# Kernel optimization log

Hardware: AMD Instinct MI355X
Metric: run time of the kernel (lower is better)

The kernel has to match this reference:

```python
import jax, jax.numpy as jnp
import numpy as np

BN_EPS = 1e-5
POOL_TARGETS = (1500, 750, 375)


def mesh_conv(x, nb, W, g, b):
    # x: (E, C), nb: (E, 4), W: (5*C, Cout)
    E, C = x.shape
    n = x[jnp.clip(nb, 0, E - 1)]              # (E, 4, C) gather
    p1 = jnp.sort(n[:, :2, :], axis=1)          # symmetrize face-pair 1
    p2 = jnp.sort(n[:, 2:, :], axis=1)          # symmetrize face-pair 2
    feat = jnp.concatenate([x, p1[:, 0], p1[:, 1], p2[:, 0], p2[:, 1]], axis=1)  # (E, 5C)
    h = feat @ W                                # (E, Cout)
    mu = h.mean(axis=0)
    var = h.var(axis=0)                         # biased var (BatchNorm training stats)
    h = (h - mu) * jax.lax.rsqrt(var + BN_EPS) * g + b
    return jax.nn.relu(h)


def mesh_pool(x, nb, target):
    E = x.shape[0]
    scores = jnp.linalg.norm(x, axis=1)
    keep = jnp.sort(jnp.argsort(-scores)[:target])          # (target,) sorted kept edges
    x_pool = x[keep]
    remap = jnp.full((E,), -1, dtype=jnp.int32).at[keep].set(jnp.arange(target, dtype=jnp.int32))
    nbr = remap[jnp.clip(nb[keep], 0, E - 1)]               # (target, 4)
    self_idx = jnp.broadcast_to(jnp.arange(target, dtype=jnp.int32)[:, None], nbr.shape)
    nb_pool = jnp.where(nbr < 0, self_idx, nbr)
    return x_pool, nb_pool, keep


def mesh_unpool(x_coarse, keep, E_fine):
    # keep is sorted ascending; nearest kept edge by integer index distance
    # (ties -> lower index, matching torch argmin-first semantics).
    idx = jnp.arange(E_fine)
    pos = jnp.searchsorted(keep, idx)
    K = keep.shape[0]
    left = jnp.clip(pos - 1, 0, K - 1)
    right = jnp.clip(pos, 0, K - 1)
    dl = jnp.abs(idx - keep[left])
    dr = jnp.abs(idx - keep[right])
    nn_idx = jnp.where(dl <= dr, left, right)
    return x_coarse[nn_idx]                                 # kept edges map to themselves (d=0)


def setup_inputs() -> dict:
    key = jax.random.key(0)
    ks = jax.random.split(key, 20)
    E = 200000
    x = jax.random.normal(ks[0], (E, 5), dtype=jnp.float32)
    nb = jax.random.randint(ks[1], (E, 4), 0, E, dtype=jnp.int64)

    def lin(k, cin, cout):
        return (jax.random.normal(k, (cin, cout), dtype=jnp.float32) * 0.05)

    dims = [(5, 64), (64, 128), (128, 256), (256, 512), (768, 256), (384, 128), (192, 64)]
    names = ['e1', 'e2', 'e3', 'e4', 'd3', 'd2', 'd1']
    inp = {'x': x, 'nb': nb}
    for i, ((cin, cout), nm) in enumerate(zip(dims, names)):
        inp['W_' + nm] = lin(ks[2 + i], cin * 5, cout)
        inp['g_' + nm] = jnp.ones((cout,), dtype=jnp.float32)
        inp['b_' + nm] = jnp.zeros((cout,), dtype=jnp.float32)
    inp['W_head'] = lin(ks[12], 64, 4)
    inp['bias_head'] = jnp.zeros((4,), dtype=jnp.float32)
    return inp


def _forward(x, nb,
             W_e1, g_e1, b_e1, W_e2, g_e2, b_e2, W_e3, g_e3, b_e3, W_e4, g_e4, b_e4,
             W_d3, g_d3, b_d3, W_d2, g_d2, b_d2, W_d1, g_d1, b_d1,
             W_head, bias_head):
    e1 = mesh_conv(x, nb, W_e1, g_e1, b_e1)
    e1p, nb1, keep1 = mesh_pool(e1, nb, POOL_TARGETS[0])
    e2 = mesh_conv(e1p, nb1, W_e2, g_e2, b_e2)
    e2p, nb2, keep2 = mesh_pool(e2, nb1, POOL_TARGETS[1])
    e3 = mesh_conv(e2p, nb2, W_e3, g_e3, b_e3)
    e3p, nb3, keep3 = mesh_pool(e3, nb2, POOL_TARGETS[2])
    e4 = mesh_conv(e3p, nb3, W_e4, g_e4, b_e4)
    d3 = mesh_unpool(e4, keep3, e3.shape[0])
    d3 = mesh_conv(jnp.concatenate([d3, e3], axis=1), nb2, W_d3, g_d3, b_d3)
    d2 = mesh_unpool(d3, keep2, e2.shape[0])
    d2 = mesh_conv(jnp.concatenate([d2, e2], axis=1), nb1, W_d2, g_d2, b_d2)
    d1 = mesh_unpool(d2, keep1, e1.shape[0])
    d1 = mesh_conv(jnp.concatenate([d1, e1], axis=1), nb, W_d1, g_d1, b_d1)
    return d1 @ W_head + bias_head


def reference(x, nb,
              W_e1, g_e1, b_e1, W_e2, g_e2, b_e2, W_e3, g_e3, b_e3, W_e4, g_e4, b_e4,
              W_d3, g_d3, b_d3, W_d2, g_d2, b_d2, W_d1, g_d1, b_d1,
              W_head, bias_head):
    return _forward(x, nb,
                    W_e1, g_e1, b_e1, W_e2, g_e2, b_e2, W_e3, g_e3, b_e3, W_e4, g_e4, b_e4,
                    W_d3, g_d3, b_d3, W_d2, g_d2, b_d2, W_d1, g_d1, b_d1,
                    W_head, bias_head)
```

## Files before the change

### kernel.cpp

```cpp
#include <hip/hip_runtime.h>
#include <stdint.h>

typedef unsigned long long u64;
typedef unsigned int u32;
typedef unsigned short ushort_t;

#define FI __device__ __forceinline__

static constexpr float BN_EPS_F = 1e-5f;
static constexpr int E0 = 200000;
static constexpr int T1 = 1500, T2 = 750, T3 = 375;
static constexpr int CAND_CAP = 4096;
static constexpr int NB_KEEP = (E0 + 1023) / 1024;

typedef __attribute__((ext_vector_type(8))) short short8;
typedef __attribute__((ext_vector_type(4))) float f32x4;

FI int iclampi(int v, int lo, int hi) { return v < lo ? lo : (v > hi ? hi : v); }

FI ushort_t f2b(float f) {
  u32 u = __float_as_uint(f);
  u32 r = (u + 0x7FFFu + ((u >> 16) & 1u)) >> 16;
  return (ushort_t)r;
}

FI int nearest_keep(const int* __restrict__ keep, int K, int idx) {
  int lo = 0, hi = K;
  while (lo < hi) { int mid = (lo + hi) >> 1; if (keep[mid] < idx) lo = mid + 1; else hi = mid; }
  int l = lo - 1; l = l < 0 ? 0 : (l > K - 1 ? K - 1 : l);
  int r = lo;     r = r < 0 ? 0 : (r > K - 1 ? K - 1 : r);
  int dl = idx - keep[l]; dl = dl < 0 ? -dl : dl;
  int dr = idx - keep[r]; dr = dr < 0 ? -dr : dr;
  return (dl <= dr) ? l : r;
}

FI int bsearch_eq(const int* __restrict__ keep, int K, int v) {
  int lo = 0, hi = K;
  while (lo < hi) { int mid = (lo + hi) >> 1; if (keep[mid] < v) lo = mid + 1; else hi = mid; }
  if (lo < K && keep[lo] == v) return lo;
  return -1;
}

template<int C, int Cout, int BR, int BC, int KT, int TR, int TC, int KSPLIT,
         bool FUSE_STATS>
__global__ __launch_bounds__((BR / TR) * (BC / TC))
void conv_kernel(const float* __restrict__ X,
                 const int* __restrict__ nb, int E,
                 const float* __restrict__ W,
                 float* __restrict__ H, float* __restrict__ stats)
{
  constexpr int NTH = (BR / TR) * (BC / TC);
  constexpr int VK = 5 * KT;
  constexpr int KC = C / KSPLIT;
  static_assert(KC % KT == 0, "KC % KT");

  const int row0 = blockIdx.x * BR;
  const int col0 = blockIdx.y * BC;
  const int c_begin = (KSPLIT > 1) ? (int)blockIdx.z * KC : 0;

  __shared__ float As[VK][BR];
  __shared__ float Bs[VK][BC];
  __shared__ int rowsS[5][BR];
  __shared__ float red[FUSE_STATS ? 2 * (BR / TR) * BC : 1];

  const int tid = threadIdx.x;

  for (int q = tid; q < BR; q += NTH) {
    int r = row0 + q;
    int rr[5];
    if (r < E) {
      rr[0] = r;
      #pragma unroll
      for (int j = 0; j < 4; j++) {
        int v = nb[(size_t)r * 4 + j];
        rr[1 + j] = iclampi(v, 0, E - 1);
      }
    } else {
      #pragma unroll
      for (int j = 0; j < 5; j++) rr[j] = -1;
    }
    #pragma unroll
    for (int j = 0; j < 5; j++) rowsS[j][q] = rr[j];
  }

  float acc[TR][TC];
  #pragma unroll
  for (int i = 0; i < TR; i++)
    #pragma unroll
    for (int j = 0; j < TC; j++) acc[i][j] = 0.f;

  const int tr = tid / (BC / TC);
  const int tc = tid % (BC / TC);
  const int rA = tr * TR;
  const int cB = tc * TC;

  for (int c0 = c_begin; c0 < c_begin + KC; c0 += KT) {
    __syncthreads();
    for (int q = tid; q < VK * (BC / 4); q += NTH) {
      int kk = q / (BC / 4);
      int c4 = q % (BC / 4);
      int p = kk / KT, t = kk % KT;
      float4 wv = *(const float4*)&W[(size_t)(p * C + c0 + t) * Cout + col0 + c4 * 4];
      *(float4*)&Bs[kk][c4 * 4] = wv;
    }
    for (int q = tid; q < BR * KT; q += NTH) {
      int t = q % KT, rq = q / KT;
      int c = c0 + t;
      float s0 = 0.f, a1 = 0.f, a2 = 0.f, a3 = 0.f, a4 = 0.f;
      if (rowsS[0][rq] >= 0) {
        float v0, v1, v2, v3;
        s0 = X[(size_t)rowsS[0][rq] * C + c];
        v0 = X[(size_t)rowsS[1][rq] * C + c];
        v1 = X[(size_t)rowsS[2][rq] * C + c];
        v2 = X[(size_t)rowsS[3][rq] * C + c];
        v3 = X[(size_t)rowsS[4][rq] * C + c];
        a1 = fminf(v0, v1); a2 = fmaxf(v0, v1);
        a3 = fminf(v2, v3); a4 = fmaxf(v2, v3);
      }
      As[0 * KT + t][rq] = s0;
      As[1 * KT + t][rq] = a1;
      As[2 * KT + t][rq] = a2;
      As[3 * KT + t][rq] = a3;
      As[4 * KT + t][rq] = a4;
    }
    __syncthreads();

    for (int kk = 0; kk < VK; kk++) {
      float a[TR], b[TC];
      #pragma unroll
      for (int i = 0; i < TR; i++) a[i] = As[kk][rA + i];
      #pragma unroll
      for (int j = 0; j < TC; j++) b[j] = Bs[kk][cB + j];
      #pragma unroll
      for (int i = 0; i < TR; i++)
        #pragma unroll
        for (int j = 0; j < TC; j++)
          acc[i][j] = fmaf(a[i], b[j], acc[i][j]);
    }
  }

  #pragma unroll
  for (int i = 0; i < TR; i++) {
    int r = row0 + rA + i;
    if (r < E) {
      if constexpr (KSPLIT > 1) {
        #pragma unroll
        for (int j = 0; j < TC; j++)
          atomicAdd(&H[(size_t)r * Cout + col0 + cB + j], acc[i][j]);
      } else {
        #pragma unroll
        for (int j = 0; j < TC; j += 4) {
          float4 v = make_float4(acc[i][j], acc[i][j + 1], acc[i][j + 2], acc[i][j + 3]);
          *(float4*)&H[(size_t)r * Cout + col0 + cB + j] = v;
        }
      }
    }
  }

  if constexpr (FUSE_STATS) {
    float s[TC], q2[TC];
    #pragma unroll
    for (int j = 0; j < TC; j++) { s[j] = 0.f; q2[j] = 0.f; }
    #pragma unroll
    for (int i = 0; i < TR; i++) {
      int r = row0 + rA + i;
      if (r < E) {
        #pragma unroll
        for (int j = 0; j < TC; j++) { float v = acc[i][j]; s[j] += v; q2[j] += v * v; }
      }
    }
    __syncthreads();
    float* redS = &red[0];
    float* redQ = &red[(BR / TR) * BC];
    #pragma unroll
    for (int j = 0; j < TC; j++) {
      redS[tr * BC + cB + j] = s[j];
      redQ[tr * BC + cB + j] = q2[j];
    }
    __syncthreads();
    for (int col = tid; col < BC; col += NTH) {
      float ts = 0.f, tq = 0.f;
      for (int g = 0; g < BR / TR; g++) { ts += redS[g * BC + col]; tq += redQ[g * BC + col]; }
      atomicAdd(&stats[col0 + col], ts);
      atomicAdd(&stats[Cout + col0 + col], tq);
    }
  }
}

__global__ __launch_bounds__(256, 4)
void d1_mfma_kernel(const ushort_t* __restrict__ d2b, const ushort_t* __restrict__ e1b,
                    const int* __restrict__ nn1, const int* __restrict__ nb,
                    const ushort_t* __restrict__ Wt,
                    float* __restrict__ H, float* __restrict__ stats)
{
  __shared__ int rowsD[5][128];
  __shared__ int rowsS[5][128];

  const int tid = threadIdx.x;
  const int lane = tid & 63;
  const int wv = tid >> 6;
  const int l15 = lane & 15;
  const int quad = lane >> 4;
  const int row0 = (int)blockIdx.x * 128;

  if (tid < 128) {
    int r = row0 + tid; if (r > E0 - 1) r = E0 - 1;
    int rs[5];
    rs[0] = r;
    #pragma unroll
    for (int j = 0; j < 4; j++) rs[1 + j] = iclampi((int)nb[(size_t)r * 4 + j], 0, E0 - 1);
    #pragma unroll
    for (int j = 0; j < 5; j++) { rowsS[j][tid] = rs[j]; rowsD[j][tid] = nn1[rs[j]]; }
  }
  __syncthreads();

  f32x4 acc[8];
  #pragma unroll
  for (int mi = 0; mi < 8; mi++) acc[mi] = (f32x4){0.f, 0.f, 0.f, 0.f};

  for (int cc = 0; cc < 6; cc++) {
    const bool fromD = cc < 4;
    const ushort_t* __restrict__ src = fromD ? d2b : e1b;
    const int stride = fromD ? 128 : 64;
    const int cbase = (fromD ? cc * 32 : (cc - 4) * 32) + quad * 8;

    short8 bf[5];
    #pragma unroll
    for (int p = 0; p < 5; p++)
      bf[p] = *(const short8*)&Wt[((size_t)(p * 64 + wv * 16 + l15)) * 192 + cc * 32 + quad * 8];

    #pragma unroll 2
    for (int mi = 0; mi < 8; mi++) {
      int rr = mi * 16 + l15;
      int r0, r1, r2, r3, r4;
      if (fromD) {
        r0 = rowsD[0][rr]; r1 = rowsD[1][rr]; r2 = rowsD[2][rr];
        r3 = rowsD[3][rr]; r4 = rowsD[4][rr];
      } else {
        r0 = rowsS[0][rr]; r1 = rowsS[1][rr]; r2 = rowsS[2][rr];
        r3 = rowsS[3][rr]; r4 = rowsS[4][rr];
      }
      uint4 v0 = *(const uint4*)&src[(size_t)r0 * stride + cbase];
      uint4 v1 = *(const uint4*)&src[(size_t)r1 * stride + cbase];
      uint4 v2 = *(const uint4*)&src[(size_t)r2 * stride + cbase];
      uint4 v3 = *(const uint4*)&src[(size_t)r3 * stride + cbase];
      uint4 v4 = *(const uint4*)&src[(size_t)r4 * stride + cbase];

      uint4 lo12, hi12, lo34, hi34;
      {
        const ushort_t* a = (const ushort_t*)&v1;
        const ushort_t* b = (const ushort_t*)&v2;
        ushort_t* lo = (ushort_t*)&lo12;
        ushort_t* hi = (ushort_t*)&hi12;
        #pragma unroll
        for (int i = 0; i < 8; i++) {
          ushort_t x = a[i], y = b[i];
          lo[i] = x < y ? x : y;
          hi[i] = x < y ? y : x;
        }
      }
      {
        const ushort_t* a = (const ushort_t*)&v3;
        const ushort_t* b = (const ushort_t*)&v4;
        ushort_t* lo = (ushort_t*)&lo34;
        ushort_t* hi = (ushort_t*)&hi34;
        #pragma unroll
        for (int i = 0; i < 8; i++) {
          ushort_t x = a[i], y = b[i];
          lo[i] = x < y ? x : y;
          hi[i] = x < y ? y : x;
        }
      }
      acc[mi] = __builtin_amdgcn_mfma_f32_16x16x32_bf16(*(short8*)&v0,   bf[0], acc[mi], 0, 0, 0);
      acc[mi] = __builtin_amdgcn_mfma_f32_16x16x32_bf16(*(short8*)&lo12, bf[1], acc[mi], 0, 0, 0);
      acc[mi] = __builtin_amdgcn_mfma_f32_16x16x32_bf16(*(short8*)&hi12, bf[2], acc[mi], 0, 0, 0);
      acc[mi] = __builtin_amdgcn_mfma_f32_16x16x32_bf16(*(short8*)&lo34, bf[3], acc[mi], 0, 0, 0);
      acc[mi] = __builtin_amdgcn_mfma_f32_16x16x32_bf16(*(short8*)&hi34, bf[4], acc[mi], 0, 0, 0);
    }
  }

  const int col = wv * 16 + l15;
  float s = 0.f, q = 0.f;
  #pragma unroll
  for (int mi = 0; mi < 8; mi++) {
    #pragma unroll
    for (int reg = 0; reg < 4; reg++) {
      int r = row0 + mi * 16 + quad * 4 + reg;
      if (r < E0) {
        float v = acc[mi][reg];
        H[(size_t)r * 64 + col] = v;
        s += v; q += v * v;
      }
    }
  }
  s += __shfl_xor(s, 16); q += __shfl_xor(q, 16);
  s += __shfl_xor(s, 32); q += __shfl_xor(q, 32);
  if (quad == 0) {
    atomicAdd(&stats[col], s);
    atomicAdd(&stats[64 + col], q);
  }
}

__global__ void prep_wd1_kernel(const float* __restrict__ W, ushort_t* __restrict__ Wt)
{
  int idx = (int)blockIdx.x * 256 + threadIdx.x;
  if (idx < 5 * 64 * 192) {
    int n = idx & 63;
    int k = idx >> 6;
    int p = k / 192, c = k % 192;
    Wt[((size_t)(p * 64 + n)) * 192 + c] = f2b(W[(size_t)k * 64 + n]);
  }
}

__global__ void stats_kernel(const float* __restrict__ H, int E, int Cout,
                             float* __restrict__ stats)
{
  const int RB = 64;
  int r0 = (int)blockIdx.x * RB;
  int rend = r0 + RB; if (rend > E) rend = E;
  for (int col = threadIdx.x; col < Cout; col += blockDim.x) {
    float s = 0.f, q = 0.f;
    for (int r = r0; r < rend; r++) { float v = H[(size_t)r * Cout + col]; s += v; q += v * v; }
    atomicAdd(&stats[col], s);
    atomicAdd(&stats[Cout + col], q);
  }
}

template<int Cout, bool KEYS, bool B16>
__global__ void bn_kernel(const float* __restrict__ H, const float* __restrict__ stats,
                          const float* __restrict__ g, const float* __restrict__ b,
                          int E, float* __restrict__ Out, ushort_t* __restrict__ Outb,
                          u64* __restrict__ keys)
{
  constexpr int CPL = Cout / 64;
  const int lane = threadIdx.x & 63;
  const int wid = threadIdx.x >> 6;
  const int wpb = blockDim.x >> 6;
  const float invE = 1.0f / (float)E;
  float mu[CPL], inv[CPL], gg[CPL], bb[CPL];
  #pragma unroll
  for (int u = 0; u < CPL; u++) {
    int c = lane + u * 64;
    float m = stats[c] * invE;
    float var = stats[Cout + c] * invE - m * m;
    mu[u] = m;
    inv[u] = rsqrtf(var + BN_EPS_F);
    gg[u] = g[c]; bb[u] = b[c];
  }
  for (int r = (int)blockIdx.x * wpb + wid; r < E; r += (int)gridDim.x * wpb) {
    float ss = 0.f;
    #pragma unroll
    for (int u = 0; u < CPL; u++) {
      int c = lane + u * 64;
      float v = H[(size_t)r * Cout + c];
      float o = (v - mu[u]) * inv[u] * gg[u] + bb[u];
      o = fmaxf(o, 0.f);
      Out[(size_t)r * Cout + c] = o;
      if constexpr (B16) Outb[(size_t)r * Cout + c] = f2b(o);
      ss += o * o;
    }
    if constexpr (KEYS) {
      #pragma unroll
      for (int s = 32; s > 0; s >>= 1) ss += __shfl_xor(ss, s, 64);
      if (lane == 0) {
        float sc = sqrtf(ss);
        u32 sb = __float_as_uint(sc);
        keys[r] = ((u64)sb << 32) | (u64)(0xFFFFFFFFu - (u32)r);
      }
    }
  }
}

__global__ void head_kernel(const float* __restrict__ H, const float* __restrict__ stats,
                            const float* __restrict__ g, const float* __restrict__ b,
                            const float* __restrict__ Wh, const float* __restrict__ bh,
                            int E, float* __restrict__ out)
{
  const int lane = threadIdx.x & 63;
  const int wid = threadIdx.x >> 6;
  const int wpb = blockDim.x >> 6;
  const float invE = 1.0f / (float)E;
  float m = stats[lane] * invE;
  float var = stats[64 + lane] * invE - m * m;
  float inv = rsqrtf(var + BN_EPS_F);
  float gg = g[lane], bb = b[lane];
  float4 w = *(const float4*)&Wh[lane * 4];
  float b0 = bh[0], b1 = bh[1], b2 = bh[2], b3 = bh[3];
  for (int r = (int)blockIdx.x * wpb + wid; r < E; r += (int)gridDim.x * wpb) {
    float v = H[(size_t)r * 64 + lane];
    float o = fmaxf((v - m) * inv * gg + bb, 0.f);
    float a0 = o * w.x, a1 = o * w.y, a2 = o * w.z, a3 = o * w.w;
    #pragma unroll
    for (int s = 32; s > 0; s >>= 1) {
      a0 += __shfl_xor(a0, s, 64);
      a1 += __shfl_xor(a1, s, 64);
      a2 += __shfl_xor(a2, s, 64);
      a3 += __shfl_xor(a3, s, 64);
    }
    if (lane == 0) {
      float4 ov = make_float4(a0 + b0, a1 + b1, a2 + b2, a3 + b3);
      *(float4*)&out[(size_t)r * 4] = ov;
    }
  }
}

__global__ void hist_kernel(const u64* __restrict__ keys, int E, u32* __restrict__ hist)
{
  for (int i = (int)blockIdx.x * blockDim.x + threadIdx.x; i < E;
       i += (int)gridDim.x * blockDim.x) {
    u32 bin = (u32)(keys[i] >> 44);
    atomicAdd(&hist[bin], 1u);
  }
}

__global__ void scan_kernel(const u32* __restrict__ hist, int K, u32* __restrict__ sel)
{
  __shared__ u32 csum[1024];
  __shared__ int selChunk;
  __shared__ u32 aboveChunk;
  const int tid = threadIdx.x;
  u32 s = 0;
  const u32* hp = hist + (size_t)tid * 1024;
  for (int i = 0; i < 1024; i++) s += hp[i];
  csum[tid] = s;
  __syncthreads();
  if (tid == 0) {
    u32 above = 0; int sc = 0; u32 ab = 0;
    for (int t = 1023; t >= 0; t--) {
      if (above + csum[t] >= (u32)K) { sc = t; ab = above; break; }
      above += csum[t];
    }
    selChunk = sc; aboveChunk = ab;
  }
  __syncthreads();
  if (tid == 0) {
    u32 above = aboveChunk; int sb = 0;
    const u32* hq = hist + (size_t)selChunk * 1024;
    for (int t = 1023; t >= 0; t--) {
      u32 c = hq[t];
      if (above + c >= (u32)K) { sb = t; break; }
      above += c;
    }
    sel[0] = (u32)(selChunk * 1024 + sb);
    sel[1] = above;
    sel[2] = (u32)K - above;
  }
}

__global__ void collect_kernel(const u64* __restrict__ keys, int E, const u32* __restrict__ sel,
                               u64* __restrict__ cand, u32* __restrict__ count)
{
  u32 bin = sel[0];
  for (int i = (int)blockIdx.x * blockDim.x + threadIdx.x; i < E;
       i += (int)gridDim.x * blockDim.x) {
    if ((u32)(keys[i] >> 44) == bin) {
      u32 p = atomicAdd(count, 1u);
      if (p < (u32)CAND_CAP) cand[p] = keys[i];
    }
  }
}

__global__ void thresh_kernel(const u64* __restrict__ cand, const u32* __restrict__ count,
                              const u32* __restrict__ sel, u64* __restrict__ thr)
{
  __shared__ u64 sk[CAND_CAP];
  const int tid = threadIdx.x;
  const int nth = blockDim.x;
  int n = (int)(*count > (u32)CAND_CAP ? (u32)CAND_CAP : *count);
  int n2 = 2; while (n2 < n) n2 <<= 1;
  for (int i = tid; i < n2; i += nth) sk[i] = (i < n) ? cand[i] : 0ull;
  __syncthreads();
  for (int k = 2; k <= n2; k <<= 1)
    for (int j = k >> 1; j > 0; j >>= 1) {
      for (int i = tid; i < n2; i += nth) {
        int p = i ^ j;
        if (p > i) {
          u64 a = sk[i], bb = sk[p];
          bool up = ((i & k) == 0);
          bool sw = up ? (a < bb) : (a > bb);
          if (sw) { sk[i] = bb; sk[p] = a; }
        }
      }
      __syncthreads();
    }
  if (tid == 0) {
    int kr = (int)sel[2];
    thr[0] = sk[kr - 1];
  }
}

__global__ void keep_count_kernel(const u64* __restrict__ keys, int E,
                                  const u64* __restrict__ thrp, u32* __restrict__ bcnt)
{
  const u64 thr = thrp[0];
  const int tid = threadIdx.x;
  int base = (int)blockIdx.x * 1024 + tid * 4;
  u32 c = 0;
  #pragma unroll
  for (int u = 0; u < 4; u++) {
    int i = base + u;
    if (i < E && keys[i] >= thr) c++;
  }
  __shared__ u32 sm[256];
  sm[tid] = c;
  __syncthreads();
  for (int s = 128; s > 0; s >>= 1) {
    if (tid < s) sm[tid] += sm[tid + s];
    __syncthreads();
  }
  if (tid == 0) bcnt[blockIdx.x] = sm[0];
}

__global__ void keep_scan_kernel(const u32* __restrict__ bcnt, int NB, u32* __restrict__ boffs)
{
  __shared__ u32 sm[256];
  const int tid = threadIdx.x;
  u32 v = (tid < NB) ? bcnt[tid] : 0;
  sm[tid] = v;
  __syncthreads();
  for (int off = 1; off < 256; off <<= 1) {
    u32 t = 0;
    if (tid >= off) t = sm[tid - off];
    __syncthreads();
    sm[tid] += t;
    __syncthreads();
  }
  if (tid < NB) boffs[tid] = sm[tid] - v;
}

__global__ void keep_scatter_kernel(const u64* __restrict__ keys, int E,
                                    const u64* __restrict__ thrp, const u32* __restrict__ boffs,
                                    int* __restrict__ keep, int K)
{
  const u64 thr = thrp[0];
  const int tid = threadIdx.x;
  int base = (int)blockIdx.x * 1024 + tid * 4;
  u32 f[4]; u32 c = 0;
  #pragma unroll
  for (int u = 0; u < 4; u++) {
    int i = base + u;
    f[u] = (i < E && keys[i] >= thr) ? 1u : 0u;
    c += f[u];
  }
  __shared__ u32 sm[256];
  sm[tid] = c;
  __syncthreads();
  for (int off = 1; off < 256; off <<= 1) {
    u32 t = 0;
    if (tid >= off) t = sm[tid - off];
    __syncthreads();
    sm[tid] += t;
    __syncthreads();
  }
  u32 pos = boffs[blockIdx.x] + sm[tid] - c;
  #pragma unroll
  for (int u = 0; u < 4; u++) {
    if (f[u]) {
      if (pos < (u32)K) keep[pos] = base + u;
      pos++;
    }
  }
}

template<int NPOW>
__global__ void pool_select_kernel(const u64* __restrict__ keys, int E, int K,
                                   int* __restrict__ keep)
{
  __shared__ u64 sk[NPOW];
  __shared__ int si[NPOW];
  const int tid = threadIdx.x, nth = blockDim.x;
  for (int i = tid; i < NPOW; i += nth) sk[i] = (i < E) ? keys[i] : 0ull;
  __syncthreads();
  for (int k = 2; k <= NPOW; k <<= 1)
    for (int j = k >> 1; j > 0; j >>= 1) {
      for (int i = tid; i < NPOW; i += nth) {
        int p = i ^ j;
        if (p > i) {
          u64 a = sk[i], bb = sk[p];
          bool up = ((i & k) == 0);
          bool sw = up ? (a < bb) : (a > bb);
          if (sw) { sk[i] = bb; sk[p] = a; }
        }
      }
      __syncthreads();
    }
  for (int i = tid; i < NPOW; i += nth)
    si[i] = (i < K) ? (int)(0xFFFFFFFFu - (u32)(sk[i] & 0xFFFFFFFFull)) : 0x7FFFFFFF;
  __syncthreads();
  for (int k = 2; k <= NPOW; k <<= 1)
    for (int j = k >> 1; j > 0; j >>= 1) {
      for (int i = tid; i < NPOW; i += nth) {
        int p = i ^ j;
        if (p > i) {
          int a = si[i], bb = si[p];
          bool up = ((i & k) == 0);
          bool sw = up ? (a > bb) : (a < bb);
          if (sw) { si[i] = bb; si[p] = a; }
        }
      }
      __syncthreads();
    }
  for (int i = tid; i < K; i += nth) keep[i] = si[i];
}

template<int C>
__global__ void pool_finish_kernel(const float* __restrict__ Xsrc, const int* __restrict__ nb_src,
                                   const int* __restrict__ keep, int K, int Esrc,
                                   float* __restrict__ Xp, int* __restrict__ nbp)
{
  int total = K * C;
  for (int idx = (int)blockIdx.x * blockDim.x + threadIdx.x; idx < total;
       idx += (int)gridDim.x * blockDim.x) {
    int i = idx / C, c = idx % C;
    Xp[idx] = Xsrc[(size_t)keep[i] * C + c];
  }
  for (int idx = (int)blockIdx.x * blockDim.x + threadIdx.x; idx < K * 4;
       idx += (int)gridDim.x * blockDim.x) {
    int i = idx >> 2, j = idx & 3;
    int v = nb_src[(size_t)keep[i] * 4 + j];
    v = iclampi(v, 0, Esrc - 1);
    int p = bsearch_eq(keep, K, v);
    nbp[idx] = (p < 0) ? i : p;
  }
}

__global__ void unpool_cat_kernel(const float* __restrict__ Xc, const float* __restrict__ Xs,
                                  const int* __restrict__ keep, int K, int E,
                                  int Cc, int Cs, float* __restrict__ out)
{
  int Ct = Cc + Cs;
  int total = E * Ct;
  for (int idx = (int)blockIdx.x * blockDim.x + threadIdx.x; idx < total;
       idx += (int)gridDim.x * blockDim.x) {
    int r = idx / Ct, c = idx % Ct;
    float v;
    if (c < Cc) { int nn = nearest_keep(keep, K, r); v = Xc[(size_t)nn * Cc + c]; }
    else v = Xs[(size_t)r * Cs + (c - Cc)];
    out[idx] = v;
  }
}

__global__ void nn_map_kernel(const int* __restrict__ keep, int K, int E, int* __restrict__ nn)
{
  for (int i = (int)blockIdx.x * blockDim.x + threadIdx.x; i < E;
       i += (int)gridDim.x * blockDim.x)
    nn[i] = nearest_keep(keep, K, i);
}

extern "C" void kernel_launch(void* const* d_in, const int* in_sizes, int n_in,
                              void* d_out, int out_size, void* d_ws, size_t ws_size,
                              hipStream_t stream)
{
  (void)in_sizes; (void)n_in; (void)out_size; (void)ws_size;
  const float* x     = (const float*)d_in[0];
  const int*   nb    = (const int*)d_in[1];
  const float* W_e1  = (const float*)d_in[2];
  const float* g_e1  = (const float*)d_in[3];
  const float* b_e1  = (const float*)d_in[4];
  const float* W_e2  = (const float*)d_in[5];
  const float* g_e2  = (const float*)d_in[6];
  const float* b_e2  = (const float*)d_in[7];
  const float* W_e3  = (const float*)d_in[8];
  const float* g_e3  = (const float*)d_in[9];
  const float* b_e3  = (const float*)d_in[10];
  const float* W_e4  = (const float*)d_in[11];
  const float* g_e4  = (const float*)d_in[12];
  const float* b_e4  = (const float*)d_in[13];
  const float* W_d3  = (const float*)d_in[14];
  const float* g_d3  = (const float*)d_in[15];
  const float* b_d3  = (const float*)d_in[16];
  const float* W_d2  = (const float*)d_in[17];
  const float* g_d2  = (const float*)d_in[18];
  const float* b_d2  = (const float*)d_in[19];
  const float* W_d1  = (const float*)d_in[20];
  const float* g_d1  = (const float*)d_in[21];
  const float* b_d1  = (const float*)d_in[22];
  const float* W_head = (const float*)d_in[23];
  const float* bias_head = (const float*)d_in[24];
  float* out = (float*)d_out;

  char* p = (char*)d_ws;
  auto alloc = [&](size_t bytes) -> char* {
    char* q = p; p += (bytes + 255) & ~(size_t)255; return q;
  };

  char* zz = p;
  u32*   hist  = (u32*)alloc(sizeof(u32) * (1u << 20));
  float* stats = (float*)alloc(sizeof(float) * 2 * (64 + 128 + 256 + 512 + 256 + 128 + 64));
  u32*   ctrl  = (u32*)alloc(sizeof(u32) * 16);
  u64*   thr   = (u64*)alloc(sizeof(u64) * 2);
  u32*   sel   = (u32*)alloc(sizeof(u32) * 8);
  float* H2    = (float*)alloc(sizeof(float) * T1 * 128);
  float* H3    = (float*)alloc(sizeof(float) * T2 * 256);
  float* H4    = (float*)alloc(sizeof(float) * T3 * 512);
  float* Hd3   = (float*)alloc(sizeof(float) * T2 * 256);
  float* Hd2   = (float*)alloc(sizeof(float) * T1 * 128);
  size_t zz_bytes = (size_t)(p - zz);
  u32*   bcnt  = (u32*)alloc(sizeof(u32) * 256);
  u32*   boffs = (u32*)alloc(sizeof(u32) * 256);
  float* e1    = (float*)alloc(sizeof(float) * (size_t)E0 * 64);
  u64*   keys1 = (u64*)alloc(sizeof(u64) * E0);
  u64*   cand  = (u64*)alloc(sizeof(u64) * CAND_CAP);
  int*   keep1 = (int*)alloc(sizeof(int) * T1);
  float* e1p   = (float*)alloc(sizeof(float) * T1 * 64);
  int*   nb1   = (int*)alloc(sizeof(int) * T1 * 4);
  float* e2    = (float*)alloc(sizeof(float) * T1 * 128);
  u64*   keys2 = (u64*)alloc(sizeof(u64) * T1);
  int*   keep2 = (int*)alloc(sizeof(int) * T2);
  float* e2p   = (float*)alloc(sizeof(float) * T2 * 128);
  int*   nb2   = (int*)alloc(sizeof(int) * T2 * 4);
  float* e3    = (float*)alloc(sizeof(float) * T2 * 256);
  u64*   keys3 = (u64*)alloc(sizeof(u64) * T2);
  int*   keep3 = (int*)alloc(sizeof(int) * T3);
  float* e3p   = (float*)alloc(sizeof(float) * T3 * 256);
  int*   nb3   = (int*)alloc(sizeof(int) * T3 * 4);
  float* e4    = (float*)alloc(sizeof(float) * T3 * 512);
  float* d3cat = (float*)alloc(sizeof(float) * T2 * 768);
  float* d3    = (float*)alloc(sizeof(float) * T2 * 256);
  float* d2cat = (float*)alloc(sizeof(float) * T1 * 384);
  float* d2    = (float*)alloc(sizeof(float) * T1 * 128);
  int*   nn1   = (int*)alloc(sizeof(int) * E0);
  float* Hd1   = (float*)alloc(sizeof(float) * (size_t)E0 * 64);
  ushort_t* e1b = (ushort_t*)alloc(sizeof(ushort_t) * (size_t)E0 * 64);
  ushort_t* d2b = (ushort_t*)alloc(sizeof(ushort_t) * T1 * 128);
  ushort_t* Wt  = (ushort_t*)alloc(sizeof(ushort_t) * 5 * 64 * 192);

  float* s1  = stats;
  float* s2  = s1 + 2 * 64;
  float* s3  = s2 + 2 * 128;
  float* s4  = s3 + 2 * 256;
  float* sd3 = s4 + 2 * 512;
  float* sd2 = sd3 + 2 * 256;
  float* sd1 = sd2 + 2 * 128;

  hipMemsetAsync(zz, 0, zz_bytes, stream);
  prep_wd1_kernel<<<dim3(240), 256, 0, stream>>>(W_d1, Wt);

  conv_kernel<5, 64, 128, 64, 5, 4, 8, 1, true>
      <<<dim3((E0 + 127) / 128, 1), 256, 0, stream>>>(x, nb, E0, W_e1, e1, s1);
  bn_kernel<64, true, true><<<dim3(8192), 256, 0, stream>>>(e1, s1, g_e1, b_e1, E0, e1, e1b, keys1);

  hist_kernel<<<dim3(782), 256, 0, stream>>>(keys1, E0, hist);
  scan_kernel<<<dim3(1), 1024, 0, stream>>>(hist, T1, sel);
  collect_kernel<<<dim3(782), 256, 0, stream>>>(keys1, E0, sel, cand, ctrl);
  thresh_kernel<<<dim3(1), 1024, 0, stream>>>(cand, ctrl, sel, thr);
  keep_count_kernel<<<dim3(NB_KEEP), 256, 0, stream>>>(keys1, E0, thr, bcnt);
  keep_scan_kernel<<<dim3(1), 256, 0, stream>>>(bcnt, NB_KEEP, boffs);
  keep_scatter_kernel<<<dim3(NB_KEEP), 256, 0, stream>>>(keys1, E0, thr, boffs, keep1, T1);
  pool_finish_kernel<64><<<dim3(380), 256, 0, stream>>>(e1, nb, keep1, T1, E0, e1p, nb1);

  conv_kernel<64, 128, 32, 64, 8, 2, 4, 2, false>
      <<<dim3((T1 + 31) / 32, 128 / 64, 2), 256, 0, stream>>>(e1p, nb1, T1, W_e2, H2, nullptr);
  stats_kernel<<<dim3((T1 + 63) / 64), 256, 0, stream>>>(H2, T1, 128, s2);
  bn_kernel<128, true, false><<<dim3(512), 256, 0, stream>>>(H2, s2, g_e2, b_e2, T1, e2, nullptr, keys2);
  pool_select_kernel<2048><<<dim3(1), 256, 0, stream>>>(keys2, T1, T2, keep2);
  pool_finish_kernel<128><<<dim3(380), 256, 0, stream>>>(e2, nb1, keep2, T2, T1, e2p, nb2);

  conv_kernel<128, 256, 32, 64, 8, 2, 4, 4, false>
      <<<dim3((T2 + 31) / 32, 256 / 64, 4), 256, 0, stream>>>(e2p, nb2, T2, W_e3, H3, nullptr);
  stats_kernel<<<dim3((T2 + 63) / 64), 256, 0, stream>>>(H3, T2, 256, s3);
  bn_kernel<256, true, false><<<dim3(256), 256, 0, stream>>>(H3, s3, g_e3, b_e3, T2, e3, nullptr, keys3);
  pool_select_kernel<1024><<<dim3(1), 256, 0, stream>>>(keys3, T2, T3, keep3);
  pool_finish_kernel<256><<<dim3(380), 256, 0, stream>>>(e3, nb2, keep3, T3, T2, e3p, nb3);

  conv_kernel<256, 512, 32, 64, 8, 2, 4, 4, false>
      <<<dim3((T3 + 31) / 32, 512 / 64, 4), 256, 0, stream>>>(e3p, nb3, T3, W_e4, H4, nullptr);
  stats_kernel<<<dim3((T3 + 63) / 64), 256, 0, stream>>>(H4, T3, 512, s4);
  bn_kernel<512, false, false><<<dim3(128), 256, 0, stream>>>(H4, s4, g_e4, b_e4, T3, e4, nullptr, nullptr);

  unpool_cat_kernel<<<dim3((T2 * 768 + 255) / 256), 256, 0, stream>>>(
      e4, e3, keep3, T3, T2, 512, 256, d3cat);
  conv_kernel<768, 256, 32, 64, 8, 2, 4, 8, false>
      <<<dim3((T2 + 31) / 32, 256 / 64, 8), 256, 0, stream>>>(d3cat, nb2, T2, W_d3, Hd3, nullptr);
  stats_kernel<<<dim3((T2 + 63) / 64), 256, 0, stream>>>(Hd3, T2, 256, sd3);
  bn_kernel<256, false, false><<<dim3(256), 256, 0, stream>>>(Hd3, sd3, g_d3, b_d3, T2, d3, nullptr, nullptr);

  unpool_cat_kernel<<<dim3((T1 * 384 + 255) / 256), 256, 0, stream>>>(
      d3, e2, keep2, T2, T1, 256, 128, d2cat);
  conv_kernel<384, 128, 32, 64, 8, 2, 4, 8, false>
      <<<dim3((T1 + 31) / 32, 128 / 64, 8), 256, 0, stream>>>(d2cat, nb1, T1, W_d2, Hd2, nullptr);
  stats_kernel<<<dim3((T1 + 63) / 64), 256, 0, stream>>>(Hd2, T1, 128, sd2);
  bn_kernel<128, false, true><<<dim3(512), 256, 0, stream>>>(Hd2, sd2, g_d2, b_d2, T1, d2, d2b, nullptr);

  nn_map_kernel<<<dim3(782), 256, 0, stream>>>(keep1, T1, E0, nn1);
  d1_mfma_kernel<<<dim3((E0 + 127) / 128), 256, 0, stream>>>(d2b, e1b, nn1, nb, Wt, Hd1, sd1);

  head_kernel<<<dim3(8192), 256, 0, stream>>>(Hd1, sd1, g_d1, b_d1, W_head, bias_head, E0, out);
}
```

Measured before the change: 1.164 ms.

## Retile d1 MFMA gather per wave, add dedicated e1 conv, two-level histogram scan

The d1 MFMA kernel now gives each wave its own 32 rows across all 64 output columns. Before, every wave gathered all 128 rows for only 16 columns, so the gathered neighbour rows were loaded four times per block; now each is loaded once. Weight fragments are loaded per pair and per 16-column group instead, and the launch bound drops to 2 blocks per SM to fit the larger accumulator set. A specialised e1 conv kernel builds the sorted 25-wide feature tile in shared memory with a float4 gather. The top-k histogram also keeps a coarse 1024-bin count, so the single-block scan no longer reads the whole 1M-entry histogram serially, at the cost of a second atomic per key.

```diff
diff --git a/kernel.cpp b/kernel.cpp
--- a/kernel.cpp
+++ b/kernel.cpp
@@ -187,7 +187,107 @@
   }
 }
 
-__global__ __launch_bounds__(256, 4)
+__global__ __launch_bounds__(256)
+void e1_conv_kernel(const float* __restrict__ X, const int* __restrict__ nb,
+                    const float* __restrict__ W,
+                    float* __restrict__ H, float* __restrict__ stats)
+{
+  __shared__ float As[25][128];
+  __shared__ float Bs[25][64];
+  __shared__ float red[2 * 32 * 64];
+
+  const int tid = threadIdx.x;
+  const int row0 = (int)blockIdx.x * 128;
+
+  if (tid < 128) {
+    int r = row0 + tid; if (r > E0 - 1) r = E0 - 1;
+    int rs[5];
+    rs[0] = r;
+    #pragma unroll
+    for (int j = 0; j < 4; j++) rs[1 + j] = iclampi((int)nb[(size_t)r * 4 + j], 0, E0 - 1);
+    float v[5][5];
+    #pragma unroll
+    for (int j = 0; j < 5; j++) {
+      const float* src = &X[(size_t)rs[j] * 5];
+      float4 a = *(const float4*)src;
+      v[j][0] = a.x; v[j][1] = a.y; v[j][2] = a.z; v[j][3] = a.w;
+      v[j][4] = src[4];
+    }
+    #pragma unroll
+    for (int c = 0; c < 5; c++) {
+      As[0 * 5 + c][tid] = v[0][c];
+      As[1 * 5 + c][tid] = fminf(v[1][c], v[2][c]);
+      As[2 * 5 + c][tid] = fmaxf(v[1][c], v[2][c]);
+      As[3 * 5 + c][tid] = fminf(v[3][c], v[4][c]);
+      As[4 * 5 + c][tid] = fmaxf(v[3][c], v[4][c]);
+    }
+  } else {
+    for (int q = tid - 128; q < 25 * 16; q += 128) {
+      int k = q / 16, c4 = q % 16;
+      float4 wv = *(const float4*)&W[(size_t)k * 64 + c4 * 4];
+      *(float4*)&Bs[k][c4 * 4] = wv;
+    }
+  }
+  __syncthreads();
+
+  const int tr = tid >> 3;
+  const int tc = tid & 7;
+  const int rA = tr * 4;
+  const int cB = tc * 8;
+
+  float acc[4][8];
+  #pragma unroll
+  for (int i = 0; i < 4; i++)
+    #pragma unroll
+    for (int j = 0; j < 8; j++) acc[i][j] = 0.f;
+
+  for (int k = 0; k < 25; k++) {
+    float a[4], b[8];
+    #pragma unroll
+    for (int i = 0; i < 4; i++) a[i] = As[k][rA + i];
+    #pragma unroll
+    for (int j = 0; j < 8; j++) b[j] = Bs[k][cB + j];
+    #pragma unroll
+    for (int i = 0; i < 4; i++)
+      #pragma unroll
+      for (int j = 0; j < 8; j++)
+        acc[i][j] = fmaf(a[i], b[j], acc[i][j]);
+  }
+
+  float s[8], q2[8];
+  #pragma unroll
+  for (int j = 0; j < 8; j++) { s[j] = 0.f; q2[j] = 0.f; }
+  #pragma unroll
+  for (int i = 0; i < 4; i++) {
+    int r = row0 + rA + i;
+    if (r < E0) {
+      #pragma unroll
+      for (int j = 0; j < 8; j += 4) {
+        float4 v = make_float4(acc[i][j], acc[i][j + 1], acc[i][j + 2], acc[i][j + 3]);
+        *(float4*)&H[(size_t)r * 64 + cB + j] = v;
+      }
+      #pragma unroll
+      for (int j = 0; j < 8; j++) { float v = acc[i][j]; s[j] += v; q2[j] += v * v; }
+    }
+  }
+  __syncthreads();
+  float* redS = &red[0];
+  float* redQ = &red[32 * 64];
+  #pragma unroll
+  for (int j = 0; j < 8; j++) {
+    redS[tr * 64 + cB + j] = s[j];
+    redQ[tr * 64 + cB + j] = q2[j];
+  }
+  __syncthreads();
+  for (int col = tid; col < 64; col += 256) {
+    float ts = 0.f, tq = 0.f;
+    for (int g = 0; g < 32; g++) { ts += redS[g * 64 + col]; tq += redQ[g * 64 + col]; }
+    atomicAdd(&stats[col], ts);
+    atomicAdd(&stats[64 + col], tq);
+  }
+}
+
+__global__ __launch_bounds__(256, 2)
 void d1_mfma_kernel(const ushort_t* __restrict__ d2b, const ushort_t* __restrict__ e1b,
                     const int* __restrict__ nn1, const int* __restrict__ nb,
                     const ushort_t* __restrict__ Wt,
@@ -214,9 +314,11 @@
   }
   __syncthreads();
 
-  f32x4 acc[8];
-  #pragma unroll
-  for (int mi = 0; mi < 8; mi++) acc[mi] = (f32x4){0.f, 0.f, 0.f, 0.f};
+  f32x4 acc[2][4];
+  #pragma unroll
+  for (int mi = 0; mi < 2; mi++)
+    #pragma unroll
+    for (int ni = 0; ni < 4; ni++) acc[mi][ni] = (f32x4){0.f, 0.f, 0.f, 0.f};
 
   for (int cc = 0; cc < 6; cc++) {
     const bool fromD = cc < 4;
@@ -224,14 +326,10 @@
     const int stride = fromD ? 128 : 64;
     const int cbase = (fromD ? cc * 32 : (cc - 4) * 32) + quad * 8;
 
-    short8 bf[5];
-    #pragma unroll
-    for (int p = 0; p < 5; p++)
-      bf[p] = *(const short8*)&Wt[((size_t)(p * 64 + wv * 16 + l15)) * 192 + cc * 32 + quad * 8];
-
-    #pragma unroll 2
-    for (int mi = 0; mi < 8; mi++) {
-      int rr = mi * 16 + l15;
+    short8 a[2][5];
+    #pragma unroll
+    for (int mi = 0; mi < 2; mi++) {
+      int rr = wv * 32 + mi * 16 + l15;
       int r0, r1, r2, r3, r4;
       if (fromD) {
         r0 = rowsD[0][rr]; r1 = rowsD[1][rr]; r2 = rowsD[2][rr];
@@ -248,56 +346,76 @@
 
       uint4 lo12, hi12, lo34, hi34;
       {
-        const ushort_t* a = (const ushort_t*)&v1;
-        const ushort_t* b = (const ushort_t*)&v2;
+        const ushort_t* pa = (const ushort_t*)&v1;
+        const ushort_t* pb = (const ushort_t*)&v2;
         ushort_t* lo = (ushort_t*)&lo12;
         ushort_t* hi = (ushort_t*)&hi12;
         #pragma unroll
         for (int i = 0; i < 8; i++) {
-          ushort_t x = a[i], y = b[i];
-          lo[i] = x < y ? x : y;
-          hi[i] = x < y ? y : x;
+          ushort_t xx = pa[i], yy = pb[i];
+          lo[i] = xx < yy ? xx : yy;
+          hi[i] = xx < yy ? yy : xx;
         }
       }
       {
-        const ushort_t* a = (const ushort_t*)&v3;
-        const ushort_t* b = (const ushort_t*)&v4;
+        const ushort_t* pa = (const ushort_t*)&v3;
+        const ushort_t* pb = (const ushort_t*)&v4;
         ushort_t* lo = (ushort_t*)&lo34;
         ushort_t* hi = (ushort_t*)&hi34;
         #pragma unroll
         for (int i = 0; i < 8; i++) {
-          ushort_t x = a[i], y = b[i];
-          lo[i] = x < y ? x : y;
-          hi[i] = x < y ? y : x;
+          ushort_t xx = pa[i], yy = pb[i];
+          lo[i] = xx < yy ? xx : yy;
+          hi[i] = xx < yy ? yy : xx;
         }
       }
-      acc[mi] = __builtin_amdgcn_mfma_f32_16x16x32_bf16(*(short8*)&v0,   bf[0], acc[mi], 0, 0, 0);
-      acc[mi] = __builtin_amdgcn_mfma_f32_16x16x32_bf16(*(short8*)&lo12, bf[1], acc[mi], 0, 0, 0);
-      acc[mi] = __builtin_amdgcn_mfma_f32_16x16x32_bf16(*(short8*)&hi12, bf[2], acc[mi], 0, 0, 0);
-      acc[mi] = __builtin_amdgcn_mfma_f32_16x16x32_bf16(*(short8*)&lo34, bf[3], acc[mi], 0, 0, 0);
-      acc[mi] = __builtin_amdgcn_mfma_f32_16x16x32_bf16(*(short8*)&hi34, bf[4], acc[mi], 0, 0, 0);
-    }
-  }
-
-  const int col = wv * 16 + l15;
-  float s = 0.f, q = 0.f;
-  #pragma unroll
-  for (int mi = 0; mi < 8; mi++) {
+      a[mi][0] = *(short8*)&v0;
+      a[mi][1] = *(short8*)&lo12;
+      a[mi][2] = *(short8*)&hi12;
+      a[mi][3] = *(short8*)&lo34;
+      a[mi][4] = *(short8*)&hi34;
+    }
+
+    #pragma unroll
+    for (int p = 0; p < 5; p++) {
+      short8 bf[4];
+      #pragma unroll
+      for (int ni = 0; ni < 4; ni++)
+        bf[ni] = *(const short8*)&Wt[((size_t)(p * 64 + ni * 16 + l15)) * 192 + cc * 32 + quad * 8];
+      #pragma unroll
+      for (int mi = 0; mi < 2; mi++)
+        #pragma unroll
+        for (int ni = 0; ni < 4; ni++)
+          acc[mi][ni] = __builtin_amdgcn_mfma_f32_16x16x32_bf16(a[mi][p], bf[ni], acc[mi][ni], 0, 0, 0);
+    }
+  }
+
+  float s[4] = {0.f, 0.f, 0.f, 0.f}, q[4] = {0.f, 0.f, 0.f, 0.f};
+  #pragma unroll
+  for (int mi = 0; mi < 2; mi++) {
     #pragma unroll
     for (int reg = 0; reg < 4; reg++) {
-      int r = row0 + mi * 16 + quad * 4 + reg;
+      int r = row0 + wv * 32 + mi * 16 + quad * 4 + reg;
       if (r < E0) {
-        float v = acc[mi][reg];
-        H[(size_t)r * 64 + col] = v;
-        s += v; q += v * v;
-      }
-    }
-  }
-  s += __shfl_xor(s, 16); q += __shfl_xor(q, 16);
-  s += __shfl_xor(s, 32); q += __shfl_xor(q, 32);
-  if (quad == 0) {
-    atomicAdd(&stats[col], s);
-    atomicAdd(&stats[64 + col], q);
+        #pragma unroll
+        for (int ni = 0; ni < 4; ni++) {
+          float v = acc[mi][ni][reg];
+          H[(size_t)r * 64 + ni * 16 + l15] = v;
+          s[ni] += v; q[ni] += v * v;
+        }
+      }
+    }
+  }
+  #pragma unroll
+  for (int ni = 0; ni < 4; ni++) {
+    float ts = s[ni], tq = q[ni];
+    ts += __shfl_xor(ts, 16); tq += __shfl_xor(tq, 16);
+    ts += __shfl_xor(ts, 32); tq += __shfl_xor(tq, 32);
+    if (quad == 0) {
+      int col = ni * 16 + l15;
+      atomicAdd(&stats[col], ts);
+      atomicAdd(&stats[64 + col], tq);
+    }
   }
 }
 
@@ -404,40 +522,42 @@
   }
 }
 
-__global__ void hist_kernel(const u64* __restrict__ keys, int E, u32* __restrict__ hist)
+__global__ void hist_kernel(const u64* __restrict__ keys, int E, u32* __restrict__ hist,
+                            u32* __restrict__ chist)
 {
   for (int i = (int)blockIdx.x * blockDim.x + threadIdx.x; i < E;
        i += (int)gridDim.x * blockDim.x) {
     u32 bin = (u32)(keys[i] >> 44);
     atomicAdd(&hist[bin], 1u);
-  }
-}
-
-__global__ void scan_kernel(const u32* __restrict__ hist, int K, u32* __restrict__ sel)
-{
-  __shared__ u32 csum[1024];
+    atomicAdd(&chist[bin >> 10], 1u);
+  }
+}
+
+__global__ void scan_kernel(const u32* __restrict__ hist, const u32* __restrict__ chist,
+                            int K, u32* __restrict__ sel)
+{
+  __shared__ u32 sc[1024];
+  __shared__ u32 sb2[1024];
   __shared__ int selChunk;
   __shared__ u32 aboveChunk;
   const int tid = threadIdx.x;
-  u32 s = 0;
-  const u32* hp = hist + (size_t)tid * 1024;
-  for (int i = 0; i < 1024; i++) s += hp[i];
-  csum[tid] = s;
+  sc[tid] = chist[tid];
   __syncthreads();
   if (tid == 0) {
-    u32 above = 0; int sc = 0; u32 ab = 0;
+    u32 above = 0; int scν = 0; u32 ab = 0;
     for (int t = 1023; t >= 0; t--) {
-      if (above + csum[t] >= (u32)K) { sc = t; ab = above; break; }
-      above += csum[t];
-    }
-    selChunk = sc; aboveChunk = ab;
-  }
+      if (above + sc[t] >= (u32)K) { scν = t; ab = above; break; }
+      above += sc[t];
+    }
+    selChunk = scν; aboveChunk = ab;
+  }
+  __syncthreads();
+  sb2[tid] = hist[(size_t)selChunk * 1024 + tid];
   __syncthreads();
   if (tid == 0) {
     u32 above = aboveChunk; int sb = 0;
-    const u32* hq = hist + (size_t)selChunk * 1024;
     for (int t = 1023; t >= 0; t--) {
-      u32 c = hq[t];
+      u32 c = sb2[t];
       if (above + c >= (u32)K) { sb = t; break; }
       above += c;
     }
@@ -686,6 +806,7 @@
 
   char* zz = p;
   u32*   hist  = (u32*)alloc(sizeof(u32) * (1u << 20));
+  u32*   chist = (u32*)alloc(sizeof(u32) * 1024);
   float* stats = (float*)alloc(sizeof(float) * 2 * (64 + 128 + 256 + 512 + 256 + 128 + 64));
   u32*   ctrl  = (u32*)alloc(sizeof(u32) * 16);
   u64*   thr   = (u64*)alloc(sizeof(u64) * 2);
@@ -736,12 +857,11 @@
   hipMemsetAsync(zz, 0, zz_bytes, stream);
   prep_wd1_kernel<<<dim3(240), 256, 0, stream>>>(W_d1, Wt);
 
-  conv_kernel<5, 64, 128, 64, 5, 4, 8, 1, true>
-      <<<dim3((E0 + 127) / 128, 1), 256, 0, stream>>>(x, nb, E0, W_e1, e1, s1);
+  e1_conv_kernel<<<dim3((E0 + 127) / 128), 256, 0, stream>>>(x, nb, W_e1, e1, s1);
   bn_kernel<64, true, true><<<dim3(8192), 256, 0, stream>>>(e1, s1, g_e1, b_e1, E0, e1, e1b, keys1);
 
-  hist_kernel<<<dim3(782), 256, 0, stream>>>(keys1, E0, hist);
-  scan_kernel<<<dim3(1), 1024, 0, stream>>>(hist, T1, sel);
+  hist_kernel<<<dim3(782), 256, 0, stream>>>(keys1, E0, hist, chist);
+  scan_kernel<<<dim3(1), 1024, 0, stream>>>(hist, chist, T1, sel);
   collect_kernel<<<dim3(782), 256, 0, stream>>>(keys1, E0, sel, cand, ctrl);
   thresh_kernel<<<dim3(1), 1024, 0, stream>>>(cand, ctrl, sel, thr);
   keep_count_kernel<<<dim3(NB_KEEP), 256, 0, stream>>>(keys1, E0, thr, bcnt);
```

After: 2.566 ms. +120.5%, slower.
